# Kernel tuning notes

Measured on AMD Instinct MI355X. Metric: run time of the kernel, lower is better.

Reference implementation:

```python
import jax, jax.numpy as jnp
import numpy as np

N = 8192
D_IN = 256
D_OUT = 256


def setup_inputs() -> dict:
    key = jax.random.key(0)
    k1, k2, k3 = jax.random.split(key, 3)
    input = jax.random.normal(k1, (N, D_IN), dtype=jnp.float32)
    adjacencyMatrix = jax.random.uniform(k2, (N, N), dtype=jnp.float32)
    W = jax.random.normal(k3, (D_OUT, D_IN), dtype=jnp.float32) * (1.0 / np.sqrt(D_IN))
    return {"input": input, "adjacencyMatrix": adjacencyMatrix, "W": W}


def reference(input, adjacencyMatrix, W):
    # degree^{-1/2} from row sums
    d_inv_sqrt = jnp.sum(adjacencyMatrix, axis=1) ** -0.5  # [N]
    # D^{-1/2} A D^{-1/2} as row/column scaling (same math as diag matmuls)
    A_norm = adjacencyMatrix * d_inv_sqrt[:, None] * d_inv_sqrt[None, :]  # [N, N]
    # A_norm @ X @ W^T (nn.Linear without bias)
    h = A_norm @ input            # [N, D_IN]
    return h @ W.T                # [N, D_OUT]
```

## Files before the change

kernel.cpp:

```cpp
#include <hip/hip_runtime.h>
#include <stdint.h>

#define NROWS 8192
#define KDIM  8192
#define DIN   256
#define DOUT  256

typedef __attribute__((ext_vector_type(8))) short bf16x8;
typedef __attribute__((ext_vector_type(4))) float f32x4;

__device__ __forceinline__ unsigned short f2bf(float f) {
    union { float f; unsigned u; } v; v.f = f;
    unsigned r = v.u + 0x7FFFu + ((v.u >> 16) & 1u);
    return (unsigned short)(r >> 16);
}

__device__ __forceinline__ void async_load16(const void* g, void* l) {
    __builtin_amdgcn_global_load_lds(
        (__attribute__((address_space(1))) void*)(void*)g,
        (__attribute__((address_space(3))) void*)l, 16, 0, 0);
}

template <bool STORE>
__global__ __launch_bounds__(256) void k_rowsum(const float* __restrict__ A,
                                                float* __restrict__ dis,
                                                unsigned short* __restrict__ Abf) {
    const int wave = threadIdx.x >> 6, lane = threadIdx.x & 63;
    const int row = (blockIdx.x << 2) + wave;
    const float4* rp = (const float4*)(A + (size_t)row * KDIM);
    unsigned short* op = STORE ? (Abf + (size_t)row * KDIM) : nullptr;
    float s0 = 0.f, s1 = 0.f, s2 = 0.f, s3 = 0.f;
    #pragma unroll
    for (int it = 0; it < 32; it += 4) {
        float4 v0 = rp[(it + 0) * 64 + lane];
        float4 v1 = rp[(it + 1) * 64 + lane];
        float4 v2 = rp[(it + 2) * 64 + lane];
        float4 v3 = rp[(it + 3) * 64 + lane];
        if (STORE) {
            short4 b0, b1, b2, b3;
            b0.x = (short)f2bf(v0.x); b0.y = (short)f2bf(v0.y);
            b0.z = (short)f2bf(v0.z); b0.w = (short)f2bf(v0.w);
            b1.x = (short)f2bf(v1.x); b1.y = (short)f2bf(v1.y);
            b1.z = (short)f2bf(v1.z); b1.w = (short)f2bf(v1.w);
            b2.x = (short)f2bf(v2.x); b2.y = (short)f2bf(v2.y);
            b2.z = (short)f2bf(v2.z); b2.w = (short)f2bf(v2.w);
            b3.x = (short)f2bf(v3.x); b3.y = (short)f2bf(v3.y);
            b3.z = (short)f2bf(v3.z); b3.w = (short)f2bf(v3.w);
            *(short4*)(op + ((size_t)(it + 0) * 64 + lane) * 4) = b0;
            *(short4*)(op + ((size_t)(it + 1) * 64 + lane) * 4) = b1;
            *(short4*)(op + ((size_t)(it + 2) * 64 + lane) * 4) = b2;
            *(short4*)(op + ((size_t)(it + 3) * 64 + lane) * 4) = b3;
        }
        s0 += (v0.x + v0.y) + (v0.z + v0.w);
        s1 += (v1.x + v1.y) + (v1.z + v1.w);
        s2 += (v2.x + v2.y) + (v2.z + v2.w);
        s3 += (v3.x + v3.y) + (v3.z + v3.w);
    }
    float s = (s0 + s1) + (s2 + s3);
    #pragma unroll
    for (int off = 32; off > 0; off >>= 1) s += __shfl_down(s, off, 64);
    if (lane == 0) dis[row] = rsqrtf(s);
}

__global__ __launch_bounds__(256, 2) void k_xw(const float* __restrict__ X,
                                               const float* __restrict__ W,
                                               const float* __restrict__ dis,
                                               unsigned short* __restrict__ Zst) {
    __shared__ short sX[64 * 72];
    __shared__ short sW[256 * 72];
    __shared__ float disS[64];
    const int tid = threadIdx.x;
    const int w = tid >> 6, lane = tid & 63, lm = lane & 15, lq = lane >> 4;
    const int j0 = blockIdx.x * 64;
    if (tid < 64) disS[tid] = dis[j0 + tid];
    f32x4 acc[4][4] = {};

    for (int s = 0; s < 4; ++s) {
        const int k0 = s * 64;
        #pragma unroll
        for (int i = 0; i < 4; ++i) {
            int e = tid + i * 256;
            int row = e >> 4, c4 = e & 15;
            float4 v = *(const float4*)(X + (size_t)(j0 + row) * DIN + k0 + c4 * 4);
            short4 b; b.x = (short)f2bf(v.x); b.y = (short)f2bf(v.y);
            b.z = (short)f2bf(v.z); b.w = (short)f2bf(v.w);
            *(short4*)&sX[row * 72 + c4 * 4] = b;
        }
        #pragma unroll
        for (int i = 0; i < 16; ++i) {
            int e = tid + i * 256;
            int row = e >> 4, c4 = e & 15;
            float4 v = *(const float4*)(W + (size_t)row * DIN + k0 + c4 * 4);
            short4 b; b.x = (short)f2bf(v.x); b.y = (short)f2bf(v.y);
            b.z = (short)f2bf(v.z); b.w = (short)f2bf(v.w);
            *(short4*)&sW[row * 72 + c4 * 4] = b;
        }
        __syncthreads();
        #pragma unroll
        for (int kk = 0; kk < 2; ++kk) {
            const int koff = kk * 32 + lq * 8;
            bf16x8 a[4], b[4];
            #pragma unroll
            for (int mt = 0; mt < 4; ++mt)
                a[mt] = *(const bf16x8*)&sX[(mt * 16 + lm) * 72 + koff];
            #pragma unroll
            for (int nt = 0; nt < 4; ++nt)
                b[nt] = *(const bf16x8*)&sW[(w * 64 + nt * 16 + lm) * 72 + koff];
            #pragma unroll
            for (int mt = 0; mt < 4; ++mt)
                #pragma unroll
                for (int nt = 0; nt < 4; ++nt)
                    acc[mt][nt] = __builtin_amdgcn_mfma_f32_16x16x32_bf16(
                        a[mt], b[nt], acc[mt][nt], 0, 0, 0);
        }
        __syncthreads();
    }

    #pragma unroll
    for (int mt = 0; mt < 4; ++mt)
        #pragma unroll
        for (int nt = 0; nt < 4; ++nt)
            #pragma unroll
            for (int r = 0; r < 4; ++r) {
                int jl = mt * 16 + lq * 4 + r;
                int n  = w * 64 + nt * 16 + lm;
                float v = acc[mt][nt][r] * disS[jl];
                sW[n * 72 + jl] = (short)f2bf(v);
            }
    __syncthreads();
    #pragma unroll
    for (int it = 0; it < 8; ++it) {
        int e = tid + it * 256;
        int n = e >> 3, ch = e & 7;
        bf16x8 val = *(const bf16x8*)&sW[n * 72 + ch * 8];
        *(bf16x8*)(Zst + (size_t)n * NROWS + j0 + ch * 8) = val;
    }
}

__global__ __launch_bounds__(256, 2) void k_gemm_bf(const unsigned short* __restrict__ Abf,
                                                    const unsigned short* __restrict__ Zst,
                                                    const float* __restrict__ dis,
                                                    float* __restrict__ out) {
    __shared__ short sA[64 * 64];
    __shared__ short sB[256 * 64];
    __shared__ float disS[64];
    const int tid = threadIdx.x;
    const int w = tid >> 6, lane = tid & 63, lm = lane & 15, lq = lane >> 4;
    const int m0 = blockIdx.x * 64;
    const int split = blockIdx.y;
    const int kbase = split * 2048;
    if (tid < 64) disS[tid] = dis[m0 + tid];
    f32x4 acc[4][4] = {};
    short* sBw = &sB[w * 4096];
    short* sAw = &sA[w * 1024];
    const int swz_c = (lane & 7) ^ (lane >> 3);

    for (int s = 0; s < 32; ++s) {
        const int k0 = kbase + s * 64;
        const unsigned short* gB =
            Zst + (size_t)(w * 64 + (lane >> 3)) * KDIM + k0 + swz_c * 8;
        #pragma unroll
        for (int i = 0; i < 8; ++i)
            async_load16(gB + (size_t)i * 8 * KDIM, &sBw[i * 512]);
        const unsigned short* gA =
            Abf + (size_t)(m0 + w * 16 + (lane >> 3)) * KDIM + k0 + swz_c * 8;
        #pragma unroll
        for (int i = 0; i < 2; ++i)
            async_load16(gA + (size_t)i * 8 * KDIM, &sAw[i * 512]);
        __syncthreads();
        #pragma unroll
        for (int kk = 0; kk < 2; ++kk) {
            const int cb = kk * 4 + lq;
            const int sc = cb ^ (lm & 7);
            bf16x8 a[4], b[4];
            #pragma unroll
            for (int mt = 0; mt < 4; ++mt)
                a[mt] = *(const bf16x8*)&sA[(mt * 16 + lm) * 64 + sc * 8];
            #pragma unroll
            for (int nt = 0; nt < 4; ++nt)
                b[nt] = *(const bf16x8*)&sBw[(nt * 16 + lm) * 64 + sc * 8];
            #pragma unroll
            for (int mt = 0; mt < 4; ++mt)
                #pragma unroll
                for (int nt = 0; nt < 4; ++nt)
                    acc[mt][nt] = __builtin_amdgcn_mfma_f32_16x16x32_bf16(
                        a[mt], b[nt], acc[mt][nt], 0, 0, 0);
        }
        __syncthreads();
    }

    #pragma unroll
    for (int mt = 0; mt < 4; ++mt)
        #pragma unroll
        for (int nt = 0; nt < 4; ++nt) {
            int col = w * 64 + nt * 16 + lm;
            #pragma unroll
            for (int r = 0; r < 4; ++r) {
                int rl = mt * 16 + lq * 4 + r;
                float v = acc[mt][nt][r] * disS[rl];
                out[(size_t)split * (NROWS * DOUT) + (size_t)(m0 + rl) * DOUT + col] = v;
            }
        }
}

template <bool ATOMIC>
__global__ __launch_bounds__(256, 2) void k_gemm(const float* __restrict__ A,
                                                 const unsigned short* __restrict__ Zst,
                                                 const float* __restrict__ dis,
                                                 float* __restrict__ out) {
    __shared__ short sA[64 * 72];
    __shared__ short sB[256 * 64];
    __shared__ float disS[64];
    const int tid = threadIdx.x;
    const int w = tid >> 6, lane = tid & 63, lm = lane & 15, lq = lane >> 4;
    const int m0 = blockIdx.x * 64;
    const int split = blockIdx.y;
    const int kbase = split * 2048;
    if (tid < 64) disS[tid] = dis[m0 + tid];
    f32x4 acc[4][4] = {};
    short* sBw = &sB[w * 4096];
    const int arow = tid >> 4, ac4 = tid & 15;
    const int swz_c = (lane & 7) ^ (lane >> 3);

    for (int s = 0; s < 32; ++s) {
        const int k0 = kbase + s * 64;
        const unsigned short* gB =
            Zst + (size_t)(w * 64 + (lane >> 3)) * KDIM + k0 + swz_c * 8;
        #pragma unroll
        for (int i = 0; i < 8; ++i)
            async_load16(gB + (size_t)i * 8 * KDIM, &sBw[i * 512]);
        #pragma unroll
        for (int i = 0; i < 4; ++i) {
            int row = arow + i * 16;
            float4 v = *(const float4*)(A + (size_t)(m0 + row) * KDIM + k0 + ac4 * 4);
            short4 b; b.x = (short)f2bf(v.x); b.y = (short)f2bf(v.y);
            b.z = (short)f2bf(v.z); b.w = (short)f2bf(v.w);
            *(short4*)&sA[row * 72 + ac4 * 4] = b;
        }
        __syncthreads();
        #pragma unroll
        for (int kk = 0; kk < 2; ++kk) {
            const int koff = kk * 32 + lq * 8;
            const int cb = kk * 4 + lq;
            bf16x8 a[4], b[4];
            #pragma unroll
            for (int mt = 0; mt < 4; ++mt)
                a[mt] = *(const bf16x8*)&sA[(mt * 16 + lm) * 72 + koff];
            #pragma unroll
            for (int nt = 0; nt < 4; ++nt) {
                int nl = nt * 16 + lm;
                int scb = cb ^ (lm & 7);
                b[nt] = *(const bf16x8*)&sBw[nl * 64 + scb * 8];
            }
            #pragma unroll
            for (int mt = 0; mt < 4; ++mt)
                #pragma unroll
                for (int nt = 0; nt < 4; ++nt)
                    acc[mt][nt] = __builtin_amdgcn_mfma_f32_16x16x32_bf16(
                        a[mt], b[nt], acc[mt][nt], 0, 0, 0);
        }
        __syncthreads();
    }

    #pragma unroll
    for (int mt = 0; mt < 4; ++mt)
        #pragma unroll
        for (int nt = 0; nt < 4; ++nt) {
            int col = w * 64 + nt * 16 + lm;
            #pragma unroll
            for (int r = 0; r < 4; ++r) {
                int rl = mt * 16 + lq * 4 + r;
                float v = acc[mt][nt][r] * disS[rl];
                if (ATOMIC) {
                    atomicAdd(out + (size_t)(m0 + rl) * DOUT + col, v);
                } else {
                    out[(size_t)split * (NROWS * DOUT) + (size_t)(m0 + rl) * DOUT + col] = v;
                }
            }
        }
}

__global__ __launch_bounds__(256) void k_reduce(const float4* __restrict__ p,
                                                float4* __restrict__ out) {
    const size_t i = (size_t)blockIdx.x * 256 + threadIdx.x;
    const size_t stride = (size_t)NROWS * DOUT / 4;
    float4 a = p[i], b = p[i + stride], c = p[i + 2 * stride], d = p[i + 3 * stride];
    float4 r;
    r.x = (a.x + b.x) + (c.x + d.x);
    r.y = (a.y + b.y) + (c.y + d.y);
    r.z = (a.z + b.z) + (c.z + d.z);
    r.w = (a.w + b.w) + (c.w + d.w);
    out[i] = r;
}

extern "C" void kernel_launch(void* const* d_in, const int* in_sizes, int n_in,
                              void* d_out, int out_size, void* d_ws, size_t ws_size,
                              hipStream_t stream) {
    const float* X = (const float*)d_in[0];
    const float* A = (const float*)d_in[1];
    const float* W = (const float*)d_in[2];
    float* out = (float*)d_out;
    char* ws = (char*)d_ws;
    float* dis = (float*)ws;
    unsigned short* Zst = (unsigned short*)(ws + 32768);
    float* part = (float*)(ws + 32768 + 4194304);
    unsigned short* Abf = (unsigned short*)(ws + 32768 + 4194304 + 33554432);
    const size_t need_mid  = 32768 + 4194304 + 4ull * NROWS * DOUT * sizeof(float);
    const size_t need_full = need_mid + (size_t)NROWS * KDIM * sizeof(unsigned short);

    if (ws_size >= need_full) {
        k_rowsum<true><<<NROWS / 4, 256, 0, stream>>>(A, dis, Abf);
        k_xw<<<NROWS / 64, 256, 0, stream>>>(X, W, dis, Zst);
        k_gemm_bf<<<dim3(NROWS / 64, 4), 256, 0, stream>>>(Abf, Zst, dis, part);
        k_reduce<<<(NROWS * DOUT / 4) / 256, 256, 0, stream>>>((const float4*)part,
                                                               (float4*)out);
    } else if (ws_size >= need_mid) {
        k_rowsum<false><<<NROWS / 4, 256, 0, stream>>>(A, dis, nullptr);
        k_xw<<<NROWS / 64, 256, 0, stream>>>(X, W, dis, Zst);
        k_gemm<false><<<dim3(NROWS / 64, 4), 256, 0, stream>>>(A, Zst, dis, part);
        k_reduce<<<(NROWS * DOUT / 4) / 256, 256, 0, stream>>>((const float4*)part,
                                                               (float4*)out);
    } else {
        k_rowsum<false><<<NROWS / 4, 256, 0, stream>>>(A, dis, nullptr);
        k_xw<<<NROWS / 64, 256, 0, stream>>>(X, W, dis, Zst);
        hipMemsetAsync(d_out, 0, (size_t)out_size * sizeof(float), stream);
        k_gemm<true><<<dim3(NROWS / 64, 4), 256, 0, stream>>>(A, Zst, dis, out);
    }
}
```

Measured before the change: 461.1 us.

## Drop bf16 copy of A; use double-buffered 128-row GEMM reading fp32 A

Removes the pass that wrote a bf16 copy of the adjacency matrix in the row-sum kernel. The main GEMM now reads fp32 A directly and converts it in registers. It uses a new 512-thread kernel with 128-row tiles, double-buffered LDS for A and B, and prefetches the next K slice while computing the current one. This avoids writing and rereading a 128MB intermediate and halves how often Z is reloaded per row tile. The cost is twice the LDS per block and fp32 A traffic inside the GEMM, which may lower occupancy.

```diff
diff --git a/kernel.cpp b/kernel.cpp
--- a/kernel.cpp
+++ b/kernel.cpp
@@ -21,14 +21,11 @@
         (__attribute__((address_space(3))) void*)l, 16, 0, 0);
 }
 
-template <bool STORE>
 __global__ __launch_bounds__(256) void k_rowsum(const float* __restrict__ A,
-                                                float* __restrict__ dis,
-                                                unsigned short* __restrict__ Abf) {
+                                                float* __restrict__ dis) {
     const int wave = threadIdx.x >> 6, lane = threadIdx.x & 63;
     const int row = (blockIdx.x << 2) + wave;
     const float4* rp = (const float4*)(A + (size_t)row * KDIM);
-    unsigned short* op = STORE ? (Abf + (size_t)row * KDIM) : nullptr;
     float s0 = 0.f, s1 = 0.f, s2 = 0.f, s3 = 0.f;
     #pragma unroll
     for (int it = 0; it < 32; it += 4) {
@@ -36,21 +33,6 @@
         float4 v1 = rp[(it + 1) * 64 + lane];
         float4 v2 = rp[(it + 2) * 64 + lane];
         float4 v3 = rp[(it + 3) * 64 + lane];
-        if (STORE) {
-            short4 b0, b1, b2, b3;
-            b0.x = (short)f2bf(v0.x); b0.y = (short)f2bf(v0.y);
-            b0.z = (short)f2bf(v0.z); b0.w = (short)f2bf(v0.w);
-            b1.x = (short)f2bf(v1.x); b1.y = (short)f2bf(v1.y);
-            b1.z = (short)f2bf(v1.z); b1.w = (short)f2bf(v1.w);
-            b2.x = (short)f2bf(v2.x); b2.y = (short)f2bf(v2.y);
-            b2.z = (short)f2bf(v2.z); b2.w = (short)f2bf(v2.w);
-            b3.x = (short)f2bf(v3.x); b3.y = (short)f2bf(v3.y);
-            b3.z = (short)f2bf(v3.z); b3.w = (short)f2bf(v3.w);
-            *(short4*)(op + ((size_t)(it + 0) * 64 + lane) * 4) = b0;
-            *(short4*)(op + ((size_t)(it + 1) * 64 + lane) * 4) = b1;
-            *(short4*)(op + ((size_t)(it + 2) * 64 + lane) * 4) = b2;
-            *(short4*)(op + ((size_t)(it + 3) * 64 + lane) * 4) = b3;
-        }
         s0 += (v0.x + v0.y) + (v0.z + v0.w);
         s1 += (v1.x + v1.y) + (v1.z + v1.w);
         s2 += (v2.x + v2.y) + (v2.z + v2.w);
@@ -137,139 +119,104 @@
     }
 }
 
-__global__ __launch_bounds__(256, 2) void k_gemm_bf(const unsigned short* __restrict__ Abf,
-                                                    const unsigned short* __restrict__ Zst,
-                                                    const float* __restrict__ dis,
-                                                    float* __restrict__ out) {
-    __shared__ short sA[64 * 64];
-    __shared__ short sB[256 * 64];
-    __shared__ float disS[64];
+template <bool ATOMIC>
+__global__ __launch_bounds__(512, 2) void k_gemm2(const float* __restrict__ A,
+                                                  const unsigned short* __restrict__ Zst,
+                                                  const float* __restrict__ dis,
+                                                  float* __restrict__ out) {
+    __shared__ short sA[2][128 * 72];
+    __shared__ short sB[2][256 * 64];
+    __shared__ float disS[128];
     const int tid = threadIdx.x;
     const int w = tid >> 6, lane = tid & 63, lm = lane & 15, lq = lane >> 4;
-    const int m0 = blockIdx.x * 64;
+    const int wm = w >> 2, wn = w & 3;
+    const int m0 = blockIdx.x * 128;
     const int split = blockIdx.y;
     const int kbase = split * 2048;
-    if (tid < 64) disS[tid] = dis[m0 + tid];
+    if (tid < 128) disS[tid] = dis[m0 + tid];
     f32x4 acc[4][4] = {};
-    short* sBw = &sB[w * 4096];
-    short* sAw = &sA[w * 1024];
     const int swz_c = (lane & 7) ^ (lane >> 3);
-
-    for (int s = 0; s < 32; ++s) {
-        const int k0 = kbase + s * 64;
-        const unsigned short* gB =
-            Zst + (size_t)(w * 64 + (lane >> 3)) * KDIM + k0 + swz_c * 8;
-        #pragma unroll
-        for (int i = 0; i < 8; ++i)
-            async_load16(gB + (size_t)i * 8 * KDIM, &sBw[i * 512]);
-        const unsigned short* gA =
-            Abf + (size_t)(m0 + w * 16 + (lane >> 3)) * KDIM + k0 + swz_c * 8;
-        #pragma unroll
-        for (int i = 0; i < 2; ++i)
-            async_load16(gA + (size_t)i * 8 * KDIM, &sAw[i * 512]);
+    const int arow = tid >> 4, ac = tid & 15;
+    float4 va[4];
+
+#define LOAD_A(K0)                                                                   \
+    do {                                                                             \
+        _Pragma("unroll")                                                            \
+        for (int i = 0; i < 4; ++i)                                                  \
+            va[i] = *(const float4*)(A + (size_t)(m0 + arow + i * 32) * KDIM + (K0) + ac * 4); \
+    } while (0)
+
+#define WRITE_A(BUF)                                                                 \
+    do {                                                                             \
+        _Pragma("unroll")                                                            \
+        for (int i = 0; i < 4; ++i) {                                                \
+            short4 b; b.x = (short)f2bf(va[i].x); b.y = (short)f2bf(va[i].y);        \
+            b.z = (short)f2bf(va[i].z); b.w = (short)f2bf(va[i].w);                  \
+            *(short4*)&sA[BUF][(arow + i * 32) * 72 + ac * 4] = b;                   \
+        }                                                                            \
+    } while (0)
+
+#define STAGE_B(BUF, K0)                                                             \
+    do {                                                                             \
+        const unsigned short* gB =                                                   \
+            Zst + (size_t)(w * 32 + (lane >> 3)) * KDIM + (K0) + swz_c * 8;          \
+        short* dst = &sB[BUF][w * 2048];                                             \
+        _Pragma("unroll")                                                            \
+        for (int i = 0; i < 4; ++i)                                                  \
+            async_load16(gB + (size_t)i * 8 * KDIM, dst + i * 512);                  \
+    } while (0)
+
+#define COMPUTE(BUF)                                                                 \
+    do {                                                                             \
+        _Pragma("unroll")                                                            \
+        for (int kk = 0; kk < 2; ++kk) {                                             \
+            const int sc = (kk * 4 + lq) ^ (lm & 7);                                 \
+            bf16x8 a[4], b[4];                                                       \
+            _Pragma("unroll")                                                        \
+            for (int mt = 0; mt < 4; ++mt)                                           \
+                a[mt] = *(const bf16x8*)&sA[BUF][(wm * 64 + mt * 16 + lm) * 72 + kk * 32 + lq * 8]; \
+            _Pragma("unroll")                                                        \
+            for (int nt = 0; nt < 4; ++nt)                                           \
+                b[nt] = *(const bf16x8*)&sB[BUF][(wn * 64 + nt * 16 + lm) * 64 + sc * 8]; \
+            _Pragma("unroll")                                                        \
+            for (int mt = 0; mt < 4; ++mt)                                           \
+                _Pragma("unroll")                                                    \
+                for (int nt = 0; nt < 4; ++nt)                                       \
+                    acc[mt][nt] = __builtin_amdgcn_mfma_f32_16x16x32_bf16(           \
+                        a[mt], b[nt], acc[mt][nt], 0, 0, 0);                         \
+        }                                                                            \
+    } while (0)
+
+    LOAD_A(kbase);
+    STAGE_B(0, kbase);
+    WRITE_A(0);
+    __syncthreads();
+
+    int cur = 0;
+    for (int s = 0; s < 31; ++s) {
+        const int kn = kbase + (s + 1) * 64;
+        LOAD_A(kn);
+        STAGE_B(cur ^ 1, kn);
+        COMPUTE(cur);
+        WRITE_A(cur ^ 1);
         __syncthreads();
-        #pragma unroll
-        for (int kk = 0; kk < 2; ++kk) {
-            const int cb = kk * 4 + lq;
-            const int sc = cb ^ (lm & 7);
-            bf16x8 a[4], b[4];
-            #pragma unroll
-            for (int mt = 0; mt < 4; ++mt)
-                a[mt] = *(const bf16x8*)&sA[(mt * 16 + lm) * 64 + sc * 8];
-            #pragma unroll
-            for (int nt = 0; nt < 4; ++nt)
-                b[nt] = *(const bf16x8*)&sBw[(nt * 16 + lm) * 64 + sc * 8];
-            #pragma unroll
-            for (int mt = 0; mt < 4; ++mt)
-                #pragma unroll
-                for (int nt = 0; nt < 4; ++nt)
-                    acc[mt][nt] = __builtin_amdgcn_mfma_f32_16x16x32_bf16(
-                        a[mt], b[nt], acc[mt][nt], 0, 0, 0);
-        }
-        __syncthreads();
-    }
+        cur ^= 1;
+    }
+    COMPUTE(cur);
+
+#undef LOAD_A
+#undef WRITE_A
+#undef STAGE_B
+#undef COMPUTE
 
     #pragma unroll
     for (int mt = 0; mt < 4; ++mt)
         #pragma unroll
         for (int nt = 0; nt < 4; ++nt) {
-            int col = w * 64 + nt * 16 + lm;
+            int col = wn * 64 + nt * 16 + lm;
             #pragma unroll
             for (int r = 0; r < 4; ++r) {
-                int rl = mt * 16 + lq * 4 + r;
-                float v = acc[mt][nt][r] * disS[rl];
-                out[(size_t)split * (NROWS * DOUT) + (size_t)(m0 + rl) * DOUT + col] = v;
-            }
-        }
-}
-
-template <bool ATOMIC>
-__global__ __launch_bounds__(256, 2) void k_gemm(const float* __restrict__ A,
-                                                 const unsigned short* __restrict__ Zst,
-                                                 const float* __restrict__ dis,
-                                                 float* __restrict__ out) {
-    __shared__ short sA[64 * 72];
-    __shared__ short sB[256 * 64];
-    __shared__ float disS[64];
-    const int tid = threadIdx.x;
-    const int w = tid >> 6, lane = tid & 63, lm = lane & 15, lq = lane >> 4;
-    const int m0 = blockIdx.x * 64;
-    const int split = blockIdx.y;
-    const int kbase = split * 2048;
-    if (tid < 64) disS[tid] = dis[m0 + tid];
-    f32x4 acc[4][4] = {};
-    short* sBw = &sB[w * 4096];
-    const int arow = tid >> 4, ac4 = tid & 15;
-    const int swz_c = (lane & 7) ^ (lane >> 3);
-
-    for (int s = 0; s < 32; ++s) {
-        const int k0 = kbase + s * 64;
-        const unsigned short* gB =
-            Zst + (size_t)(w * 64 + (lane >> 3)) * KDIM + k0 + swz_c * 8;
-        #pragma unroll
-        for (int i = 0; i < 8; ++i)
-            async_load16(gB + (size_t)i * 8 * KDIM, &sBw[i * 512]);
-        #pragma unroll
-        for (int i = 0; i < 4; ++i) {
-            int row = arow + i * 16;
-            float4 v = *(const float4*)(A + (size_t)(m0 + row) * KDIM + k0 + ac4 * 4);
-            short4 b; b.x = (short)f2bf(v.x); b.y = (short)f2bf(v.y);
-            b.z = (short)f2bf(v.z); b.w = (short)f2bf(v.w);
-            *(short4*)&sA[row * 72 + ac4 * 4] = b;
-        }
-        __syncthreads();
-        #pragma unroll
-        for (int kk = 0; kk < 2; ++kk) {
-            const int koff = kk * 32 + lq * 8;
-            const int cb = kk * 4 + lq;
-            bf16x8 a[4], b[4];
-            #pragma unroll
-            for (int mt = 0; mt < 4; ++mt)
-                a[mt] = *(const bf16x8*)&sA[(mt * 16 + lm) * 72 + koff];
-            #pragma unroll
-            for (int nt = 0; nt < 4; ++nt) {
-                int nl = nt * 16 + lm;
-                int scb = cb ^ (lm & 7);
-                b[nt] = *(const bf16x8*)&sBw[nl * 64 + scb * 8];
-            }
-            #pragma unroll
-            for (int mt = 0; mt < 4; ++mt)
-                #pragma unroll
-                for (int nt = 0; nt < 4; ++nt)
-                    acc[mt][nt] = __builtin_amdgcn_mfma_f32_16x16x32_bf16(
-                        a[mt], b[nt], acc[mt][nt], 0, 0, 0);
-        }
-        __syncthreads();
-    }
-
-    #pragma unroll
-    for (int mt = 0; mt < 4; ++mt)
-        #pragma unroll
-        for (int nt = 0; nt < 4; ++nt) {
-            int col = w * 64 + nt * 16 + lm;
-            #pragma unroll
-            for (int r = 0; r < 4; ++r) {
-                int rl = mt * 16 + lq * 4 + r;
+                int rl = wm * 64 + mt * 16 + lq * 4 + r;
                 float v = acc[mt][nt][r] * disS[rl];
                 if (ATOMIC) {
                     atomicAdd(out + (size_t)(m0 + rl) * DOUT + col, v);
@@ -304,26 +251,16 @@
     float* dis = (float*)ws;
     unsigned short* Zst = (unsigned short*)(ws + 32768);
     float* part = (float*)(ws + 32768 + 4194304);
-    unsigned short* Abf = (unsigned short*)(ws + 32768 + 4194304 + 33554432);
-    const size_t need_mid  = 32768 + 4194304 + 4ull * NROWS * DOUT * sizeof(float);
-    const size_t need_full = need_mid + (size_t)NROWS * KDIM * sizeof(unsigned short);
-
-    if (ws_size >= need_full) {
-        k_rowsum<true><<<NROWS / 4, 256, 0, stream>>>(A, dis, Abf);
-        k_xw<<<NROWS / 64, 256, 0, stream>>>(X, W, dis, Zst);
-        k_gemm_bf<<<dim3(NROWS / 64, 4), 256, 0, stream>>>(Abf, Zst, dis, part);
-        k_reduce<<<(NROWS * DOUT / 4) / 256, 256, 0, stream>>>((const float4*)part,
-                                                               (float4*)out);
-    } else if (ws_size >= need_mid) {
-        k_rowsum<false><<<NROWS / 4, 256, 0, stream>>>(A, dis, nullptr);
-        k_xw<<<NROWS / 64, 256, 0, stream>>>(X, W, dis, Zst);
-        k_gemm<false><<<dim3(NROWS / 64, 4), 256, 0, stream>>>(A, Zst, dis, part);
+    const size_t need = 32768 + 4194304 + 4ull * NROWS * DOUT * sizeof(float);
+
+    k_rowsum<<<NROWS / 4, 256, 0, stream>>>(A, dis);
+    k_xw<<<NROWS / 64, 256, 0, stream>>>(X, W, dis, Zst);
+    if (ws_size >= need) {
+        k_gemm2<false><<<dim3(NROWS / 128, 4), 512, 0, stream>>>(A, Zst, dis, part);
         k_reduce<<<(NROWS * DOUT / 4) / 256, 256, 0, stream>>>((const float4*)part,
                                                                (float4*)out);
     } else {
-        k_rowsum<false><<<NROWS / 4, 256, 0, stream>>>(A, dis, nullptr);
-        k_xw<<<NROWS / 64, 256, 0, stream>>>(X, W, dis, Zst);
         hipMemsetAsync(d_out, 0, (size_t)out_size * sizeof(float), stream);
-        k_gemm<true><<<dim3(NROWS / 64, 4), 256, 0, stream>>>(A, Zst, dis, out);
-    }
-}
+        k_gemm2<true><<<dim3(NROWS / 128, 4), 512, 0, stream>>>(A, Zst, dis, out);
+    }
+}
```

Result: faster. 448.9 us (-2.6%).
